# Optimization experiments

Measured on AMD Instinct MI355X. Metric: run time of the kernel, lower is better.

Reference implementation:

```python
import jax, jax.numpy as jnp
import numpy as np

# LinearQuantWLog hyperparameters (from init_kwargs)
GAMMA = 2.0
INIT = 0.25
SIZE = 5
N_TOKENS = 262144
IN_FEATURES = 256
OUT_FEATURES = 256


def exp_proj(w):
    """Project weights onto the logarithmic grid {sign(w) * INIT * GAMMA**k, k=0..SIZE-1}.

    Mirrors elastic_quant_connect.exp_proj used by QuantLogDense: round the
    base-GAMMA log of |w|/INIT, clamp the exponent to [0, SIZE-1].
    """
    log_g = jnp.log(jnp.abs(w) / INIT) / jnp.log(GAMMA)
    k = jnp.clip(jnp.round(log_g), 0.0, SIZE - 1.0)  # -inf at w==0 clips to 0; sign(0)=0 kills it
    return jnp.sign(w) * (INIT * jnp.power(GAMMA, k))


def setup_inputs() -> dict:
    key = jax.random.key(0)
    k_in, k_w = jax.random.split(key)
    wmax = INIT * GAMMA ** (SIZE - 1)  # reset_parameters uniform range
    inputs = {
        "input": jax.random.normal(k_in, (N_TOKENS, IN_FEATURES), dtype=jnp.float32),
        "weight": jax.random.uniform(k_w, (OUT_FEATURES, IN_FEATURES), dtype=jnp.float32,
                                     minval=-wmax, maxval=wmax),
        "bias": jnp.zeros((OUT_FEATURES,), dtype=jnp.float32),
    }
    return inputs


def reference(input, weight, bias):
    # Quantize weights to the log grid, then dense matmul (F.linear semantics).
    w_q = exp_proj(weight)  # [out, in]
    return jnp.dot(input, w_q.T) + bias  # [N, out]
```

## Files before the change

### kernel.cpp

```cpp
#include <hip/hip_runtime.h>
#include <hip/hip_bf16.h>
#include <stdint.h>

typedef float  f32x4  __attribute__((ext_vector_type(4)));
typedef __bf16 bf16x8 __attribute__((ext_vector_type(8)));
typedef unsigned int u32;
typedef u32 u32v2 __attribute__((ext_vector_type(2)));

#define GRID   1024
#define MROWS  32
#define ITERS  8
#define TILEB  (MROWS * 1024)
#define WSB    65536

__device__ __forceinline__ float qlog(float v) {
    float a = fabsf(v);
    int k = (a >= 0.35355339059327373f)
          + (a >= 0.70710678118654746f)
          + (a >= 1.41421356237309515f)
          + (a >= 2.82842712474619029f);
    float q = 0.25f * (float)(1 << k);
    return (v == 0.0f) ? 0.0f : copysignf(q, v);
}

__device__ __forceinline__ u32 enc1(float q) {
    u32 b16 = __float_as_uint(q) >> 16;
    return b16 ? (((b16 >> 8) & 0x80u) | (((b16 >> 7) & 0xFFu) - 64u)) : 0u;
}
__device__ __forceinline__ u32 dec2(u32 d) {
    u32 t = d & 0x00800080u;
    return (d + t + 0x00400040u) << 7;
}
__device__ __forceinline__ bf16x8 dec_frag(u32 c0, u32 c1) {
#if __has_builtin(__builtin_amdgcn_perm)
    u32 d0 = __builtin_amdgcn_perm(0u, c0, 0x0C010C00u);
    u32 d1 = __builtin_amdgcn_perm(0u, c0, 0x0C030C02u);
    u32 d2 = __builtin_amdgcn_perm(0u, c1, 0x0C010C00u);
    u32 d3 = __builtin_amdgcn_perm(0u, c1, 0x0C030C02u);
#else
    u32 d0 = (c0 & 0xFFu) | ((c0 & 0xFF00u) << 8);
    u32 d1 = ((c0 >> 16) & 0xFFu) | ((c0 & 0xFF000000u) >> 8);
    u32 d2 = (c1 & 0xFFu) | ((c1 & 0xFF00u) << 8);
    u32 d3 = ((c1 >> 16) & 0xFFu) | ((c1 & 0xFF000000u) >> 8);
#endif
    union { u32 u[4]; bf16x8 v; } u_;
    u_.u[0] = dec2(d0); u_.u[1] = dec2(d1);
    u_.u[2] = dec2(d2); u_.u[3] = dec2(d3);
    return u_.v;
}

__device__ __forceinline__ void gload16(const float* g, char* l) {
#if __has_builtin(__builtin_amdgcn_global_load_lds)
    __builtin_amdgcn_global_load_lds(
        (const __attribute__((address_space(1))) u32*)g,
        (__attribute__((address_space(3))) u32*)l, 16, 0, 0);
#else
    const int lane = threadIdx.x & 63;
    *(f32x4*)(l + lane * 16) = *(const f32x4*)(g + lane * 4);
#endif
}

__global__ __launch_bounds__(256) void lqw_quant(
    const float* __restrict__ w, u32v2* __restrict__ wsq)
{
    const int gid  = blockIdx.x * 256 + threadIdx.x;
    const int lane = gid & 63;
    const int kt   = (gid >> 6) & 7;
    const int ntv  = gid >> 9;
    const float* src = w + (size_t)(ntv * 16 + (lane & 15)) * 256
                         + kt * 32 + (lane >> 4) * 8;
    u32v2 c = (u32v2){0, 0};
    #pragma unroll
    for (int e = 0; e < 4; ++e) c[0] |= enc1(qlog(src[e]))     << (8 * e);
    #pragma unroll
    for (int e = 0; e < 4; ++e) c[1] |= enc1(qlog(src[4 + e])) << (8 * e);
    wsq[gid] = c;
    __threadfence();
}

template<bool USE_WS>
__global__ __launch_bounds__(512, 4) void lqw_gemm(
    const float* __restrict__ in,
    const float* __restrict__ w,
    const float* __restrict__ bias,
    const u32v2* __restrict__ wsq,
    float* __restrict__ out)
{
    __shared__ __align__(16) char smem[2 * TILEB];
    const int tid  = threadIdx.x;
    const int lane = tid & 63;
    const int wv   = tid >> 6;
    const int nbase = wv * 32;
    const int lrow = lane & 15;
    const int kgrp = lane >> 4;
    const int s    = lrow & 7;
    const int o0 = ((kgrp * 2)     ^ s) * 16;
    const int o1 = ((kgrp * 2 + 1) ^ s) * 16;

    u32v2 bc[2][8];
    if (USE_WS) {
        #pragma unroll
        for (int nt = 0; nt < 2; ++nt)
            #pragma unroll
            for (int kt = 0; kt < 8; ++kt)
                bc[nt][kt] = wsq[(size_t)((wv * 2 + nt) * 8 + kt) * 64 + lane];
    } else {
        #pragma unroll
        for (int nt = 0; nt < 2; ++nt) {
            const float* wrow = w + (size_t)(nbase + nt * 16 + lrow) * 256;
            #pragma unroll
            for (int kt = 0; kt < 8; ++kt) {
                u32v2 c = (u32v2){0, 0};
                #pragma unroll
                for (int e = 0; e < 4; ++e)
                    c[0] |= enc1(qlog(wrow[kt * 32 + kgrp * 8 + e])) << (8 * e);
                #pragma unroll
                for (int e = 0; e < 4; ++e)
                    c[1] |= enc1(qlog(wrow[kt * 32 + kgrp * 8 + 4 + e])) << (8 * e);
                bc[nt][kt] = c;
            }
        }
    }
    f32x4 bv[2];
    #pragma unroll
    for (int nt = 0; nt < 2; ++nt)
        bv[nt] = *(const f32x4*)(bias + nbase + nt * 16 + kgrp * 4);

    const int mt0 = blockIdx.x * ITERS;

    #define STAGE(b, mt) do {                                               \
        char* _d = smem + (b) * TILEB;                                      \
        _Pragma("unroll")                                                   \
        for (int j = 0; j < 4; ++j) {                                       \
            const int r = wv * 4 + j;                                       \
            const float* _s = in + ((size_t)(mt) * MROWS + r) * 256         \
                                 + ((lane ^ (r & 7)) << 2);                 \
            gload16(_s, _d + r * 1024);                                     \
        }                                                                   \
    } while (0)

    #define COMPUTE(b, mt) do {                                                             \
        const char* base = smem + (b) * TILEB;                                              \
        f32x4 acc[2][2];                                                                    \
        _Pragma("unroll")                                                                   \
        for (int mi = 0; mi < 2; ++mi)                                                      \
            _Pragma("unroll")                                                               \
            for (int nt = 0; nt < 2; ++nt) acc[mi][nt] = bv[nt];                            \
        const char* row0 = base + (size_t)lrow * 1024;                                      \
        const char* row1 = base + (size_t)(16 + lrow) * 1024;                               \
        _Pragma("unroll")                                                                   \
        for (int kt = 0; kt < 8; ++kt) {                                                    \
            f32x4 lo0 = *(const f32x4*)(row0 + kt * 128 + o0);                              \
            f32x4 hi0 = *(const f32x4*)(row0 + kt * 128 + o1);                              \
            f32x4 lo1 = *(const f32x4*)(row1 + kt * 128 + o0);                              \
            f32x4 hi1 = *(const f32x4*)(row1 + kt * 128 + o1);                              \
            bf16x8 a0, a1;                                                                  \
            _Pragma("unroll")                                                               \
            for (int e = 0; e < 4; ++e) {                                                   \
                a0[e] = (__bf16)lo0[e]; a0[4 + e] = (__bf16)hi0[e];                         \
                a1[e] = (__bf16)lo1[e]; a1[4 + e] = (__bf16)hi1[e];                         \
            }                                                                               \
            bf16x8 b0 = dec_frag(bc[0][kt][0], bc[0][kt][1]);                               \
            bf16x8 b1 = dec_frag(bc[1][kt][0], bc[1][kt][1]);                               \
            acc[0][0] = __builtin_amdgcn_mfma_f32_16x16x32_bf16(b0, a0, acc[0][0], 0, 0, 0); \
            acc[0][1] = __builtin_amdgcn_mfma_f32_16x16x32_bf16(b1, a0, acc[0][1], 0, 0, 0); \
            acc[1][0] = __builtin_amdgcn_mfma_f32_16x16x32_bf16(b0, a1, acc[1][0], 0, 0, 0); \
            acc[1][1] = __builtin_amdgcn_mfma_f32_16x16x32_bf16(b1, a1, acc[1][1], 0, 0, 0); \
        }                                                                                   \
        _Pragma("unroll")                                                                   \
        for (int mi = 0; mi < 2; ++mi) {                                                    \
            float* orow = out + (size_t)((mt) * MROWS + mi * 16 + lrow) * 256 + nbase + kgrp * 4; \
            *(f32x4*)(orow)      = acc[mi][0];                                              \
            *(f32x4*)(orow + 16) = acc[mi][1];                                              \
        }                                                                                   \
    } while (0)

    STAGE(0, mt0);
    asm volatile("s_waitcnt vmcnt(0)" ::: "memory");
    __builtin_amdgcn_s_barrier();

    #pragma unroll 1
    for (int t = 0; t < ITERS; ++t) {
        const int b = t & 1;
        if (t + 1 < ITERS) STAGE(b ^ 1, mt0 + t + 1);
        __builtin_amdgcn_sched_barrier(0);
        COMPUTE(b, mt0 + t);
        asm volatile("s_waitcnt vmcnt(4) lgkmcnt(0)" ::: "memory");
        __builtin_amdgcn_sched_barrier(0);
        __builtin_amdgcn_s_barrier();
    }
}

extern "C" void kernel_launch(void* const* d_in, const int* in_sizes, int n_in,
                              void* d_out, int out_size, void* d_ws, size_t ws_size,
                              hipStream_t stream) {
    const float* in_p   = (const float*)d_in[0];
    const float* w_p    = (const float*)d_in[1];
    const float* bias_p = (const float*)d_in[2];
    float* out_p        = (float*)d_out;
    if (ws_size >= WSB) {
        u32v2* wsq = (u32v2*)d_ws;
        lqw_quant<<<32, 256, 0, stream>>>(w_p, wsq);
        lqw_gemm<true><<<GRID, 512, 0, stream>>>(in_p, w_p, bias_p, wsq, out_p);
    } else {
        lqw_gemm<false><<<GRID, 512, 0, stream>>>(in_p, w_p, bias_p, nullptr, out_p);
    }
}
```

Measured before the change: 115.6 us.

## Deepen input prefetch to four-buffer ring with smaller 16-row tiles

Halves the row tile from 32 to 16 and doubles the iterations per block. It replaces the double buffer with a four-slot LDS ring that prefetches three tiles ahead, keeping total LDS the same. The aim is to keep more global loads in flight and hide memory latency in this bandwidth-bound GEMM. In exchange, each tile carries less MFMA work and the barrier count doubles. The fixed vmcnt(6) wait may under-wait in the last iterations, when no new stage is issued.

```diff
diff --git a/kernel.cpp b/kernel.cpp
--- a/kernel.cpp
+++ b/kernel.cpp
@@ -8,9 +8,10 @@
 typedef u32 u32v2 __attribute__((ext_vector_type(2)));
 
 #define GRID   1024
-#define MROWS  32
-#define ITERS  8
-#define TILEB  (MROWS * 1024)
+#define TROWS  16
+#define ITERS  16
+#define TILEB  (TROWS * 1024)
+#define NBUF   4
 #define WSB    65536
 
 __device__ __forceinline__ float qlog(float v) {
@@ -86,7 +87,7 @@
     const u32v2* __restrict__ wsq,
     float* __restrict__ out)
 {
-    __shared__ __align__(16) char smem[2 * TILEB];
+    __shared__ __align__(16) char smem[NBUF * TILEB];
     const int tid  = threadIdx.x;
     const int lane = tid & 63;
     const int wv   = tid >> 6;
@@ -128,64 +129,50 @@
 
     const int mt0 = blockIdx.x * ITERS;
 
-    #define STAGE(b, mt) do {                                               \
-        char* _d = smem + (b) * TILEB;                                      \
+    #define STAGE(bi, mt) do {                                              \
+        char* _d = smem + (bi) * TILEB;                                     \
         _Pragma("unroll")                                                   \
-        for (int j = 0; j < 4; ++j) {                                       \
-            const int r = wv * 4 + j;                                       \
-            const float* _s = in + ((size_t)(mt) * MROWS + r) * 256         \
+        for (int j = 0; j < 2; ++j) {                                       \
+            const int r = wv * 2 + j;                                       \
+            const float* _s = in + ((size_t)(mt) * TROWS + r) * 256         \
                                  + ((lane ^ (r & 7)) << 2);                 \
             gload16(_s, _d + r * 1024);                                     \
         }                                                                   \
     } while (0)
 
-    #define COMPUTE(b, mt) do {                                                             \
-        const char* base = smem + (b) * TILEB;                                              \
-        f32x4 acc[2][2];                                                                    \
-        _Pragma("unroll")                                                                   \
-        for (int mi = 0; mi < 2; ++mi)                                                      \
-            _Pragma("unroll")                                                               \
-            for (int nt = 0; nt < 2; ++nt) acc[mi][nt] = bv[nt];                            \
-        const char* row0 = base + (size_t)lrow * 1024;                                      \
-        const char* row1 = base + (size_t)(16 + lrow) * 1024;                               \
+    #define COMPUTE(bi, mt) do {                                                            \
+        const char* row0 = smem + (bi) * TILEB + (size_t)lrow * 1024;                       \
+        f32x4 acc[2];                                                                       \
+        acc[0] = bv[0]; acc[1] = bv[1];                                                     \
         _Pragma("unroll")                                                                   \
         for (int kt = 0; kt < 8; ++kt) {                                                    \
-            f32x4 lo0 = *(const f32x4*)(row0 + kt * 128 + o0);                              \
-            f32x4 hi0 = *(const f32x4*)(row0 + kt * 128 + o1);                              \
-            f32x4 lo1 = *(const f32x4*)(row1 + kt * 128 + o0);                              \
-            f32x4 hi1 = *(const f32x4*)(row1 + kt * 128 + o1);                              \
-            bf16x8 a0, a1;                                                                  \
+            f32x4 lo = *(const f32x4*)(row0 + kt * 128 + o0);                               \
+            f32x4 hi = *(const f32x4*)(row0 + kt * 128 + o1);                               \
+            bf16x8 a0;                                                                      \
             _Pragma("unroll")                                                               \
-            for (int e = 0; e < 4; ++e) {                                                   \
-                a0[e] = (__bf16)lo0[e]; a0[4 + e] = (__bf16)hi0[e];                         \
-                a1[e] = (__bf16)lo1[e]; a1[4 + e] = (__bf16)hi1[e];                         \
-            }                                                                               \
+            for (int e = 0; e < 4; ++e) { a0[e] = (__bf16)lo[e]; a0[4 + e] = (__bf16)hi[e]; } \
             bf16x8 b0 = dec_frag(bc[0][kt][0], bc[0][kt][1]);                               \
             bf16x8 b1 = dec_frag(bc[1][kt][0], bc[1][kt][1]);                               \
-            acc[0][0] = __builtin_amdgcn_mfma_f32_16x16x32_bf16(b0, a0, acc[0][0], 0, 0, 0); \
-            acc[0][1] = __builtin_amdgcn_mfma_f32_16x16x32_bf16(b1, a0, acc[0][1], 0, 0, 0); \
-            acc[1][0] = __builtin_amdgcn_mfma_f32_16x16x32_bf16(b0, a1, acc[1][0], 0, 0, 0); \
-            acc[1][1] = __builtin_amdgcn_mfma_f32_16x16x32_bf16(b1, a1, acc[1][1], 0, 0, 0); \
+            acc[0] = __builtin_amdgcn_mfma_f32_16x16x32_bf16(b0, a0, acc[0], 0, 0, 0);      \
+            acc[1] = __builtin_amdgcn_mfma_f32_16x16x32_bf16(b1, a0, acc[1], 0, 0, 0);      \
         }                                                                                   \
-        _Pragma("unroll")                                                                   \
-        for (int mi = 0; mi < 2; ++mi) {                                                    \
-            float* orow = out + (size_t)((mt) * MROWS + mi * 16 + lrow) * 256 + nbase + kgrp * 4; \
-            *(f32x4*)(orow)      = acc[mi][0];                                              \
-            *(f32x4*)(orow + 16) = acc[mi][1];                                              \
-        }                                                                                   \
+        float* orow = out + (size_t)((mt) * TROWS + lrow) * 256 + nbase + kgrp * 4;         \
+        *(f32x4*)(orow)      = acc[0];                                                      \
+        *(f32x4*)(orow + 16) = acc[1];                                                      \
     } while (0)
 
     STAGE(0, mt0);
-    asm volatile("s_waitcnt vmcnt(0)" ::: "memory");
+    STAGE(1, mt0 + 1);
+    STAGE(2, mt0 + 2);
+    asm volatile("s_waitcnt vmcnt(4)" ::: "memory");
     __builtin_amdgcn_s_barrier();
 
     #pragma unroll 1
     for (int t = 0; t < ITERS; ++t) {
-        const int b = t & 1;
-        if (t + 1 < ITERS) STAGE(b ^ 1, mt0 + t + 1);
+        if (t + 3 < ITERS) STAGE((t + 3) & (NBUF - 1), mt0 + t + 3);
         __builtin_amdgcn_sched_barrier(0);
-        COMPUTE(b, mt0 + t);
-        asm volatile("s_waitcnt vmcnt(4) lgkmcnt(0)" ::: "memory");
+        COMPUTE(t & (NBUF - 1), mt0 + t);
+        asm volatile("s_waitcnt vmcnt(6) lgkmcnt(0)" ::: "memory");
         __builtin_amdgcn_sched_barrier(0);
         __builtin_amdgcn_s_barrier();
     }
```

Result: no change. 115.5 us (-0.1%).
